# Kernel tuning notes

Hardware: AMD Instinct MI355X
Metric: run time of the kernel (lower is better)

Reference implementation:

```python
import jax, jax.numpy as jnp
import numpy as np

B, H, W, C = 64, 32, 32, 256
HZ, WZ = 16, 16
N = 64          # hidden_dim = n_proposals
K = 3           # dynamic depthwise kernel size
EPS = 1e-5


def _layernorm(x, g, b):
    mu = jnp.mean(x, axis=-1, keepdims=True)
    var = jnp.var(x, axis=-1, keepdims=True)
    return (x - mu) * jax.lax.rsqrt(var + EPS) * g + b


def setup_inputs() -> dict:
    key = jax.random.key(0)
    ks = jax.random.split(key, 8)
    s = 0.02  # weight init scale
    return {
        "x_feat": jax.random.normal(ks[0], (B, H, W, C), jnp.float32),
        "z_feat": jax.random.normal(ks[1], (B, HZ, WZ, C), jnp.float32),
        "Wz": jax.random.normal(ks[2], (C, N), jnp.float32) * s,
        "bz": jnp.zeros((N,), jnp.float32),
        "Wx": jax.random.normal(ks[3], (C, N), jnp.float32) * s,
        "bx": jnp.zeros((N,), jnp.float32),
        "Wdyn": jax.random.normal(ks[4], (C, N + K), jnp.float32) * s,
        "bdyn": jnp.zeros((N + K,), jnp.float32),
        "g_norm": jnp.ones((C,), jnp.float32),
        "b_norm": jnp.zeros((C,), jnp.float32),
        "Wp": jax.random.normal(ks[5], (C, 1), jnp.float32) * s,
        "bp": jnp.zeros((1,), jnp.float32),
        "g_ln": jnp.ones((C,), jnp.float32),
        "b_ln": jnp.zeros((C,), jnp.float32),
    }


def _dysep_conv_atten(query, value, Wdyn, bdyn, g_norm, b_norm):
    # query, value: [B, N, C]
    dy = query @ Wdyn + bdyn                      # [B, N, N+K]
    w_depth = dy[:, :, :K]                        # [B, N, K] per-channel depthwise kernels
    w_point = dy[:, :, K:]                        # [B, N, N] per-sample pointwise (1x1) weights
    # depthwise conv along C with 'same' padding (torch conv1d = cross-correlation)
    vpad = jnp.pad(value, ((0, 0), (0, 0), (1, 1)))
    depth = (w_depth[..., 0:1] * vpad[:, :, 0:C]
             + w_depth[..., 1:2] * vpad[:, :, 1:C + 1]
             + w_depth[..., 2:3] * vpad[:, :, 2:C + 2])
    depth = jax.nn.relu(depth)                    # [B, N, C]
    point = jnp.einsum('bnm,bmc->bnc', w_point, depth)
    return _layernorm(point, g_norm, b_norm)


def reference(x_feat, z_feat, Wz, bz, Wx, bx, Wdyn, bdyn,
              g_norm, b_norm, Wp, bp, g_ln, b_ln):
    # kernels from template features (detached in the original: kernels.detach())
    z_core = z_feat @ Wz + bz                                   # [B,HZ,WZ,N]
    kernels = jnp.einsum('bhwn,bhwc->bnc', z_core, z_feat)      # [B,N,C]
    kernels = jax.lax.stop_gradient(kernels)

    x_n = x_feat @ Wx + bx                                      # [B,H,W,N]
    kernels_x = jnp.einsum('bhwn,bhwc->bnc', x_n, x_feat)       # [B,N,C]
    kernels_x = _dysep_conv_atten(kernels, kernels_x, Wdyn, bdyn, g_norm, b_norm)

    x_corr = jnp.einsum('bnc,bhwn->bhwc', kernels_x, x_n)       # [B,H,W,C]
    proto = kernels_x @ Wp + bp                                 # [B,N,1]
    tem = jax.nn.sigmoid(jnp.einsum('bnd,bnc->bdc', proto, kernels_x))  # [B,1,C]
    tem = tem[:, :, None, :]                                    # [B,1,1,C]
    x_corr = x_corr * tem

    return x_feat + jax.nn.relu(_layernorm(x_corr, g_ln, b_ln))
```

## Files before the change

kernel.cpp:

```cpp
#include <hip/hip_runtime.h>
#include <math.h>

#define EPSV 1e-5f

__global__ __launch_bounds__(256) void gemm_all(
    const float* __restrict__ Xx, const float* __restrict__ Wxp,
    const float* __restrict__ bxp, float* __restrict__ Yx,
    const float* __restrict__ Xz, const float* __restrict__ Wzp,
    const float* __restrict__ bzp, float* __restrict__ Yz)
{
    __shared__ float Xc[16 * 132];
    __shared__ float Wc[16 * 64];
    const int t = threadIdx.x;
    const float *X, *W, *bias; float* Y; long r0;
    if (blockIdx.x < 512) { X = Xx; W = Wxp; bias = bxp; Y = Yx; r0 = (long)blockIdx.x * 128; }
    else                  { X = Xz; W = Wzp; bias = bzp; Y = Yz; r0 = (long)(blockIdx.x - 512) * 128; }

    const int tr = t >> 4, tc = t & 15;
    float4 bv = *(const float4*)(bias + tc * 4);
    float acc[8][4];
#pragma unroll
    for (int i = 0; i < 8; ++i) { acc[i][0]=bv.x; acc[i][1]=bv.y; acc[i][2]=bv.z; acc[i][3]=bv.w; }

    const int lr = t >> 2;
    const int lc = (t & 3) * 4;
    const int wl = t >> 4, wj = (t & 15) * 4;
    float4 xv0 = *(const float4*)(X + (r0 + lr) * 256 + lc);
    float4 xv1 = *(const float4*)(X + (r0 + lr + 64) * 256 + lc);
    float4 wv  = *(const float4*)(W + (long)wl * 64 + wj);

    for (int c0 = 0; c0 < 256; c0 += 16) {
        Xc[(lc+0)*132 + lr] = xv0.x; Xc[(lc+1)*132 + lr] = xv0.y;
        Xc[(lc+2)*132 + lr] = xv0.z; Xc[(lc+3)*132 + lr] = xv0.w;
        Xc[(lc+0)*132 + lr+64] = xv1.x; Xc[(lc+1)*132 + lr+64] = xv1.y;
        Xc[(lc+2)*132 + lr+64] = xv1.z; Xc[(lc+3)*132 + lr+64] = xv1.w;
        *(float4*)&Wc[wl * 64 + wj] = wv;
        __syncthreads();
        if (c0 + 16 < 256) {
            xv0 = *(const float4*)(X + (r0 + lr) * 256 + c0 + 16 + lc);
            xv1 = *(const float4*)(X + (r0 + lr + 64) * 256 + c0 + 16 + lc);
            wv  = *(const float4*)(W + (long)(c0 + 16 + wl) * 64 + wj);
        }
#pragma unroll
        for (int cl = 0; cl < 16; ++cl) {
            float4 a0 = *(float4*)&Xc[cl * 132 + tr * 8];
            float4 a1 = *(float4*)&Xc[cl * 132 + tr * 8 + 4];
            float4 b4 = *(float4*)&Wc[cl * 64 + tc * 4];
            acc[0][0]+=a0.x*b4.x; acc[0][1]+=a0.x*b4.y; acc[0][2]+=a0.x*b4.z; acc[0][3]+=a0.x*b4.w;
            acc[1][0]+=a0.y*b4.x; acc[1][1]+=a0.y*b4.y; acc[1][2]+=a0.y*b4.z; acc[1][3]+=a0.y*b4.w;
            acc[2][0]+=a0.z*b4.x; acc[2][1]+=a0.z*b4.y; acc[2][2]+=a0.z*b4.z; acc[2][3]+=a0.z*b4.w;
            acc[3][0]+=a0.w*b4.x; acc[3][1]+=a0.w*b4.y; acc[3][2]+=a0.w*b4.z; acc[3][3]+=a0.w*b4.w;
            acc[4][0]+=a1.x*b4.x; acc[4][1]+=a1.x*b4.y; acc[4][2]+=a1.x*b4.z; acc[4][3]+=a1.x*b4.w;
            acc[5][0]+=a1.y*b4.x; acc[5][1]+=a1.y*b4.y; acc[5][2]+=a1.y*b4.z; acc[5][3]+=a1.y*b4.w;
            acc[6][0]+=a1.z*b4.x; acc[6][1]+=a1.z*b4.y; acc[6][2]+=a1.z*b4.z; acc[6][3]+=a1.z*b4.w;
            acc[7][0]+=a1.w*b4.x; acc[7][1]+=a1.w*b4.y; acc[7][2]+=a1.w*b4.z; acc[7][3]+=a1.w*b4.w;
        }
        __syncthreads();
    }
#pragma unroll
    for (int i = 0; i < 8; ++i) {
        float4 o = make_float4(acc[i][0], acc[i][1], acc[i][2], acc[i][3]);
        *(float4*)(Y + (r0 + tr * 8 + i) * 64 + tc * 4) = o;
    }
}

__global__ __launch_bounds__(256) void corr_all(
    const float* __restrict__ xn, const float* __restrict__ xf,
    float* __restrict__ kxr, const float* __restrict__ zc,
    const float* __restrict__ zf, float* __restrict__ kern)
{
    __shared__ float A[64 * 64];
    __shared__ float Bt[64 * 64];
    const int t = threadIdx.x;
    const float *Yn, *X; float* S; int b, P;
    if (blockIdx.y < 64) { b = blockIdx.y;      Yn = xn; X = xf; S = kxr;  P = 1024; }
    else                 { b = blockIdx.y - 64; Yn = zc; X = zf; S = kern; P = 256;  }
    const int c0 = blockIdx.x * 64;
    const int tn = t >> 4, tc = t & 15;

    float acc[4][4] = {};
    float4 av[4], bv4[4];
#pragma unroll
    for (int i = 0; i < 4; ++i) {
        int idx = t + i * 256; int p = idx >> 4, f4 = (idx & 15) * 4;
        long rb = (long)b * P + p;
        av[i]  = *(const float4*)(Yn + rb * 64 + f4);
        bv4[i] = *(const float4*)(X + rb * 256 + c0 + f4);
    }
    for (int p0 = 0; p0 < P; p0 += 64) {
#pragma unroll
        for (int i = 0; i < 4; ++i) {
            int idx = t + i * 256; int p = idx >> 4, f4 = (idx & 15) * 4;
            *(float4*)&A[p * 64 + f4] = av[i];
            *(float4*)&Bt[p * 64 + f4] = bv4[i];
        }
        __syncthreads();
        if (p0 + 64 < P) {
#pragma unroll
            for (int i = 0; i < 4; ++i) {
                int idx = t + i * 256; int p = idx >> 4, f4 = (idx & 15) * 4;
                long rb = (long)b * P + p0 + 64 + p;
                av[i]  = *(const float4*)(Yn + rb * 64 + f4);
                bv4[i] = *(const float4*)(X + rb * 256 + c0 + f4);
            }
        }
#pragma unroll 16
        for (int p = 0; p < 64; ++p) {
            float4 a  = *(float4*)&A[p * 64 + tn * 4];
            float4 b4 = *(float4*)&Bt[p * 64 + tc * 4];
            acc[0][0]+=a.x*b4.x; acc[0][1]+=a.x*b4.y; acc[0][2]+=a.x*b4.z; acc[0][3]+=a.x*b4.w;
            acc[1][0]+=a.y*b4.x; acc[1][1]+=a.y*b4.y; acc[1][2]+=a.y*b4.z; acc[1][3]+=a.y*b4.w;
            acc[2][0]+=a.z*b4.x; acc[2][1]+=a.z*b4.y; acc[2][2]+=a.z*b4.z; acc[2][3]+=a.z*b4.w;
            acc[3][0]+=a.w*b4.x; acc[3][1]+=a.w*b4.y; acc[3][2]+=a.w*b4.z; acc[3][3]+=a.w*b4.w;
        }
        __syncthreads();
    }
#pragma unroll
    for (int i = 0; i < 4; ++i) {
        float4 o = make_float4(acc[i][0], acc[i][1], acc[i][2], acc[i][3]);
        *(float4*)(S + ((long)(b * 64 + tn * 4 + i)) * 256 + c0 + tc * 4) = o;
    }
}

__global__ __launch_bounds__(256) void dy_all(
    const float* __restrict__ kern, const float* __restrict__ Wdyn,
    const float* __restrict__ bdyn, float* __restrict__ dyb)
{
    __shared__ float Ac[16 * 64];
    __shared__ float Wc[16 * 64];
    __shared__ float Wd3[48];
    const int b = blockIdx.x, t = threadIdx.x;
    const int tr = t >> 4, tc = t & 15;
    float acc[4][4];
#pragma unroll
    for (int j = 0; j < 4; ++j) {
        float bj = bdyn[3 + tc * 4 + j];
        acc[0][j] = bj; acc[1][j] = bj; acc[2][j] = bj; acc[3][j] = bj;
    }
    const int lr = t >> 2, lc = (t & 3) * 4;
    const int wl = t >> 4, wj = (t & 15) * 4;
    const int nwd = t / 3, jwd = t - nwd * 3;
    float wdacc = 0.f;
    float4 av = *(const float4*)(kern + ((long)(b * 64 + lr)) * 256 + lc);
    float w0 = Wdyn[wl * 67 + 3 + wj + 0];
    float w1 = Wdyn[wl * 67 + 3 + wj + 1];
    float w2 = Wdyn[wl * 67 + 3 + wj + 2];
    float w3 = Wdyn[wl * 67 + 3 + wj + 3];
    float wdr = (t < 48) ? Wdyn[(t / 3) * 67 + (t % 3)] : 0.f;

    for (int c0 = 0; c0 < 256; c0 += 16) {
        Ac[(lc+0)*64 + lr] = av.x; Ac[(lc+1)*64 + lr] = av.y;
        Ac[(lc+2)*64 + lr] = av.z; Ac[(lc+3)*64 + lr] = av.w;
        Wc[wl*64 + wj+0] = w0; Wc[wl*64 + wj+1] = w1;
        Wc[wl*64 + wj+2] = w2; Wc[wl*64 + wj+3] = w3;
        if (t < 48) Wd3[t] = wdr;
        __syncthreads();
        if (c0 + 16 < 256) {
            av = *(const float4*)(kern + ((long)(b * 64 + lr)) * 256 + c0 + 16 + lc);
            w0 = Wdyn[(c0 + 16 + wl) * 67 + 3 + wj + 0];
            w1 = Wdyn[(c0 + 16 + wl) * 67 + 3 + wj + 1];
            w2 = Wdyn[(c0 + 16 + wl) * 67 + 3 + wj + 2];
            w3 = Wdyn[(c0 + 16 + wl) * 67 + 3 + wj + 3];
            if (t < 48) wdr = Wdyn[(c0 + 16 + t / 3) * 67 + (t % 3)];
        }
#pragma unroll
        for (int cl = 0; cl < 16; ++cl) {
            float4 a = *(float4*)&Ac[cl * 64 + tr * 4];
            float4 w = *(float4*)&Wc[cl * 64 + tc * 4];
            acc[0][0]+=a.x*w.x; acc[0][1]+=a.x*w.y; acc[0][2]+=a.x*w.z; acc[0][3]+=a.x*w.w;
            acc[1][0]+=a.y*w.x; acc[1][1]+=a.y*w.y; acc[1][2]+=a.y*w.z; acc[1][3]+=a.y*w.w;
            acc[2][0]+=a.z*w.x; acc[2][1]+=a.z*w.y; acc[2][2]+=a.z*w.z; acc[2][3]+=a.z*w.w;
            acc[3][0]+=a.w*w.x; acc[3][1]+=a.w*w.y; acc[3][2]+=a.w*w.z; acc[3][3]+=a.w*w.w;
        }
        if (t < 192) {
#pragma unroll
            for (int cl = 0; cl < 16; ++cl)
                wdacc += Ac[cl * 64 + nwd] * Wd3[cl * 3 + jwd];
        }
        __syncthreads();
    }
#pragma unroll
    for (int i = 0; i < 4; ++i) {
        float4 o = make_float4(acc[i][0], acc[i][1], acc[i][2], acc[i][3]);
        *(float4*)(dyb + ((long)(b * 64 + tr * 4 + i)) * 68 + tc * 4) = o;
    }
    if (t < 192) dyb[((long)(b * 64 + nwd)) * 68 + 64 + jwd] = wdacc + bdyn[jwd];
}

__global__ __launch_bounds__(256) void depthpoint(
    const float* __restrict__ dyb, const float* __restrict__ v,
    const float* __restrict__ g, const float* __restrict__ Wp,
    float* __restrict__ point, float* __restrict__ partials)
{
    __shared__ float smem[13312];
    float* wpT = smem;
    float* wd3 = smem + 4352;
    float* vt  = smem + 4608;
    float* dep = smem + 8960;
    float* rs  = vt;

    const int t = threadIdx.x;
    const int b = blockIdx.y, ct = blockIdx.x, c0 = ct * 64;
    const int tr = t >> 4, tc = t & 15;

#pragma unroll
    for (int i = 0; i < 4; ++i) {
        int idx = t + i * 256; int n = idx >> 4, m0 = (idx & 15) * 4;
        float4 w4 = *(const float4*)(dyb + ((long)(b * 64 + n)) * 68 + m0);
        wpT[(m0+0)*68 + n] = w4.x; wpT[(m0+1)*68 + n] = w4.y;
        wpT[(m0+2)*68 + n] = w4.z; wpT[(m0+3)*68 + n] = w4.w;
    }
    if (t < 64) {
        long o = ((long)(b * 64 + t)) * 68 + 64;
        wd3[t*4+0] = dyb[o+0]; wd3[t*4+1] = dyb[o+1]; wd3[t*4+2] = dyb[o+2];
    }
    {
        int m = t >> 2, lc0 = (t & 3) * 17;
#pragma unroll
        for (int k = 0; k < 17; ++k) {
            int lc = lc0 + k;
            if (lc < 66) {
                int c = c0 - 1 + lc;
                vt[m * 68 + lc] = (c >= 0 && c < 256) ? v[((long)(b * 64 + m)) * 256 + c] : 0.f;
            }
        }
    }
    __syncthreads();
#pragma unroll
    for (int im = 0; im < 4; ++im) {
        int m = tr * 4 + im;
        float w0 = wd3[m*4+0], w1 = wd3[m*4+1], w2 = wd3[m*4+2];
#pragma unroll
        for (int jc = 0; jc < 4; ++jc) {
            int cl = tc * 4 + jc;
            float d = w0 * vt[m*68 + cl] + w1 * vt[m*68 + cl + 1] + w2 * vt[m*68 + cl + 2];
            dep[m*68 + cl] = fmaxf(d, 0.f);
        }
    }
    __syncthreads();
    float acc[4][4] = {};
#pragma unroll 16
    for (int m = 0; m < 64; ++m) {
        float4 a4 = *(float4*)&wpT[m * 68 + tr * 4];
        float4 d4 = *(float4*)&dep[m * 68 + tc * 4];
        acc[0][0]+=a4.x*d4.x; acc[0][1]+=a4.x*d4.y; acc[0][2]+=a4.x*d4.z; acc[0][3]+=a4.x*d4.w;
        acc[1][0]+=a4.y*d4.x; acc[1][1]+=a4.y*d4.y; acc[1][2]+=a4.y*d4.z; acc[1][3]+=a4.y*d4.w;
        acc[2][0]+=a4.z*d4.x; acc[2][1]+=a4.z*d4.y; acc[2][2]+=a4.z*d4.z; acc[2][3]+=a4.z*d4.w;
        acc[3][0]+=a4.w*d4.x; acc[3][1]+=a4.w*d4.y; acc[3][2]+=a4.w*d4.z; acc[3][3]+=a4.w*d4.w;
    }
    int cg = c0 + tc * 4;
    float4 g4  = *(const float4*)(g + cg);
    float4 wp4 = *(const float4*)(Wp + cg);
    float gw0 = g4.x*wp4.x, gw1 = g4.y*wp4.y, gw2 = g4.z*wp4.z, gw3 = g4.w*wp4.w;
#pragma unroll
    for (int i = 0; i < 4; ++i) {
        float4 o = make_float4(acc[i][0], acc[i][1], acc[i][2], acc[i][3]);
        *(float4*)(point + ((long)(b * 64 + tr * 4 + i)) * 256 + cg) = o;
        float s  = o.x + o.y + o.z + o.w;
        float s2 = o.x*o.x + o.y*o.y + o.z*o.z + o.w*o.w;
        float dg = o.x*gw0 + o.y*gw1 + o.z*gw2 + o.w*gw3;
        rs[0*1088 + (tr*4+i)*17 + tc] = s;
        rs[1*1088 + (tr*4+i)*17 + tc] = s2;
        rs[2*1088 + (tr*4+i)*17 + tc] = dg;
    }
    __syncthreads();
    if (t < 64) {
        float s = 0.f, s2 = 0.f, dg = 0.f;
#pragma unroll
        for (int j = 0; j < 16; ++j) {
            s  += rs[t*17 + j];
            s2 += rs[1088 + t*17 + j];
            dg += rs[2176 + t*17 + j];
        }
        long base = ((long)(b * 4 + ct)) * 192;
        partials[base + t]        = s;
        partials[base + 64 + t]   = s2;
        partials[base + 128 + t]  = dg;
    }
}

__global__ __launch_bounds__(256) void lntem(
    const float* __restrict__ partials, const float* __restrict__ point,
    const float* __restrict__ g, const float* __restrict__ bta,
    const float* __restrict__ Wp, const float* __restrict__ bp,
    float* __restrict__ murr, float* __restrict__ AB)
{
    __shared__ float sA[256], sB[256];
    __shared__ float wnv[64];
    __shared__ float tot[4];
    const int b = blockIdx.x, t = threadIdx.x;
    const int c = t;
    float gc = g[c], bc = bta[c], wpc = Wp[c];
    sA[t] = gc * wpc; sB[t] = bc * wpc;
    __syncthreads();
    for (int off = 128; off >= 1; off >>= 1) {
        if (t < off) { sA[t] += sA[t+off]; sB[t] += sB[t+off]; }
        __syncthreads();
    }
    if (t == 0) { tot[0] = sA[0]; tot[1] = sB[0] + bp[0]; }
    __syncthreads();
    float Sgw = tot[0], Sbw = tot[1];

    float protoe = 0.f, mu = 0.f, rr = 0.f;
    if (t < 64) {
        float S1 = 0.f, S2 = 0.f, Sdg = 0.f;
#pragma unroll
        for (int ct = 0; ct < 4; ++ct) {
            long o = ((long)(b * 4 + ct)) * 192;
            S1 += partials[o + t]; S2 += partials[o + 64 + t]; Sdg += partials[o + 128 + t];
        }
        mu = S1 * (1.f / 256.f);
        float var = S2 * (1.f / 256.f) - mu * mu;
        rr = rsqrtf(var + EPSV);
        protoe = rr * (Sdg - mu * Sgw) + Sbw;
        wnv[t] = protoe * rr;
        murr[b * 128 + 2*t]     = rr;
        murr[b * 128 + 2*t + 1] = -mu * rr;
    }
    __syncthreads();
    sA[t] = (t < 64) ? protoe * rr * mu : 0.f;
    sB[t] = (t < 64) ? protoe : 0.f;
    __syncthreads();
    for (int off = 128; off >= 1; off >>= 1) {
        if (t < off) { sA[t] += sA[t+off]; sB[t] += sB[t+off]; }
        __syncthreads();
    }
    if (t == 0) { tot[2] = sA[0]; tot[3] = sB[0]; }
    __syncthreads();
    float Bv = tot[2], Sv = tot[3];

    const float* pcol = point + (long)b * 64 * 256 + c;
    float a0 = 0.f, a1 = 0.f, a2 = 0.f, a3 = 0.f;
#pragma unroll
    for (int n = 0; n < 64; n += 4) {
        a0 += wnv[n+0] * pcol[(n+0) * 256];
        a1 += wnv[n+1] * pcol[(n+1) * 256];
        a2 += wnv[n+2] * pcol[(n+2) * 256];
        a3 += wnv[n+3] * pcol[(n+3) * 256];
    }
    float accA = a0 + a1 + a2 + a3;
    float x = gc * (accA - Bv) + bc * Sv;
    float temv = 1.f / (1.f + expf(-x));
    AB[b * 512 + c]       = gc * temv;
    AB[b * 512 + 256 + c] = bc * temv;
}

__global__ __launch_bounds__(256) void final_kernel(
    const float* __restrict__ xn, const float* __restrict__ point,
    const float* __restrict__ murr, const float* __restrict__ AB,
    const float* __restrict__ xf, const float* __restrict__ g,
    const float* __restrict__ bt, float* __restrict__ out)
{
    __shared__ float xtT[64 * 68];
    __shared__ float kc[64 * 68];
    __shared__ float rs1[64 * 17], rs2[64 * 17];
    __shared__ float mu[64], rr[64];
    __shared__ float rq[128];
    const int t = threadIdx.x;
    const int b = blockIdx.y;
    const int pg = blockIdx.x;
    const int tr = t >> 4;
    const int tc = t & 15;

    if (t < 128) rq[t] = murr[b * 128 + t];
    {
        int row = t >> 2, q = t & 3;
        const float* src = xn + ((long)(b * 1024 + pg * 64 + row)) * 64 + q * 16;
        float4 f0 = *(const float4*)(src + 0);
        float4 f1 = *(const float4*)(src + 4);
        float4 f2 = *(const float4*)(src + 8);
        float4 f3 = *(const float4*)(src + 12);
        int n0 = q * 16;
        xtT[(n0+ 0)*68+row]=f0.x; xtT[(n0+ 1)*68+row]=f0.y; xtT[(n0+ 2)*68+row]=f0.z; xtT[(n0+ 3)*68+row]=f0.w;
        xtT[(n0+ 4)*68+row]=f1.x; xtT[(n0+ 5)*68+row]=f1.y; xtT[(n0+ 6)*68+row]=f1.z; xtT[(n0+ 7)*68+row]=f1.w;
        xtT[(n0+ 8)*68+row]=f2.x; xtT[(n0+ 9)*68+row]=f2.y; xtT[(n0+10)*68+row]=f2.z; xtT[(n0+11)*68+row]=f2.w;
        xtT[(n0+12)*68+row]=f3.x; xtT[(n0+13)*68+row]=f3.y; xtT[(n0+14)*68+row]=f3.z; xtT[(n0+15)*68+row]=f3.w;
    }

    float4 xcv[4][4];
    float si[4] = {0.f,0.f,0.f,0.f}, s2i[4] = {0.f,0.f,0.f,0.f};
#pragma unroll
    for (int cc = 0; cc < 4; ++cc) {
        __syncthreads();
#pragma unroll
        for (int i = 0; i < 4; ++i) {
            int idx = t + i * 256;
            int n = idx >> 4, jq = idx & 15;
            int cb = cc * 64 + jq * 4;
            float4 p4 = *(const float4*)(point + ((long)(b * 64 + n)) * 256 + cb);
            float rn = rq[2*n], qn = rq[2*n + 1];
            float4 A4 = *(const float4*)(AB + b * 512 + cb);
            float4 B4 = *(const float4*)(AB + b * 512 + 256 + cb);
            float4 kv;
            kv.x = (p4.x * rn + qn) * A4.x + B4.x;
            kv.y = (p4.y * rn + qn) * A4.y + B4.y;
            kv.z = (p4.z * rn + qn) * A4.z + B4.z;
            kv.w = (p4.w * rn + qn) * A4.w + B4.w;
            *(float4*)&kc[n * 68 + jq * 4] = kv;
        }
        __syncthreads();
        float4 a0 = {0,0,0,0}, a1 = {0,0,0,0}, a2 = {0,0,0,0}, a3 = {0,0,0,0};
#pragma unroll 8
        for (int n = 0; n < 64; ++n) {
            float4 xv = *(float4*)&xtT[n * 68 + tr * 4];
            float4 kv = *(float4*)&kc[n * 68 + tc * 4];
            a0.x += xv.x*kv.x; a0.y += xv.x*kv.y; a0.z += xv.x*kv.z; a0.w += xv.x*kv.w;
            a1.x += xv.y*kv.x; a1.y += xv.y*kv.y; a1.z += xv.y*kv.z; a1.w += xv.y*kv.w;
            a2.x += xv.z*kv.x; a2.y += xv.z*kv.y; a2.z += xv.z*kv.z; a2.w += xv.z*kv.w;
            a3.x += xv.w*kv.x; a3.y += xv.w*kv.y; a3.z += xv.w*kv.z; a3.w += xv.w*kv.w;
        }
        xcv[cc][0] = a0; xcv[cc][1] = a1; xcv[cc][2] = a2; xcv[cc][3] = a3;
        si[0] += a0.x+a0.y+a0.z+a0.w;  s2i[0] += a0.x*a0.x+a0.y*a0.y+a0.z*a0.z+a0.w*a0.w;
        si[1] += a1.x+a1.y+a1.z+a1.w;  s2i[1] += a1.x*a1.x+a1.y*a1.y+a1.z*a1.z+a1.w*a1.w;
        si[2] += a2.x+a2.y+a2.z+a2.w;  s2i[2] += a2.x*a2.x+a2.y*a2.y+a2.z*a2.z+a2.w*a2.w;
        si[3] += a3.x+a3.y+a3.z+a3.w;  s2i[3] += a3.x*a3.x+a3.y*a3.y+a3.z*a3.z+a3.w*a3.w;
    }
#pragma unroll
    for (int i = 0; i < 4; ++i) { rs1[(tr*4+i)*17 + tc] = si[i]; rs2[(tr*4+i)*17 + tc] = s2i[i]; }
    __syncthreads();
    if (t < 64) {
        float s = 0.f, s2 = 0.f;
#pragma unroll
        for (int k = 0; k < 16; ++k) { s += rs1[t*17 + k]; s2 += rs2[t*17 + k]; }
        float m = s * (1.f / 256.f);
        mu[t] = m; rr[t] = rsqrtf(s2 * (1.f / 256.f) - m * m + EPSV);
    }
    __syncthreads();
#pragma unroll
    for (int cc = 0; cc < 4; ++cc) {
        int cb = cc * 64 + tc * 4;
        float4 g4 = *(const float4*)(g + cb);
        float4 b4 = *(const float4*)(bt + cb);
#pragma unroll
        for (int i = 0; i < 4; ++i) {
            int row = tr * 4 + i;
            float m = mu[row], r = rr[row];
            long grow = ((long)(b * 1024 + pg * 64 + row)) * 256;
            float4 xfv = *(const float4*)(xf + grow + cb);
            float4 a = xcv[cc][i];
            float4 o;
            o.x = xfv.x + fmaxf((a.x - m) * r * g4.x + b4.x, 0.f);
            o.y = xfv.y + fmaxf((a.y - m) * r * g4.y + b4.y, 0.f);
            o.z = xfv.z + fmaxf((a.z - m) * r * g4.z + b4.z, 0.f);
            o.w = xfv.w + fmaxf((a.w - m) * r * g4.w + b4.w, 0.f);
            *(float4*)(out + grow + cb) = o;
        }
    }
}

extern "C" void kernel_launch(void* const* d_in, const int* in_sizes, int n_in,
                              void* d_out, int out_size, void* d_ws, size_t ws_size,
                              hipStream_t stream)
{
    (void)in_sizes; (void)n_in; (void)out_size; (void)ws_size;
    const float* x_feat = (const float*)d_in[0];
    const float* z_feat = (const float*)d_in[1];
    const float* Wz     = (const float*)d_in[2];
    const float* bz     = (const float*)d_in[3];
    const float* Wx     = (const float*)d_in[4];
    const float* bx     = (const float*)d_in[5];
    const float* Wdyn   = (const float*)d_in[6];
    const float* bdyn   = (const float*)d_in[7];
    const float* g_norm = (const float*)d_in[8];
    const float* b_norm = (const float*)d_in[9];
    const float* Wp     = (const float*)d_in[10];
    const float* bp     = (const float*)d_in[11];
    const float* g_ln   = (const float*)d_in[12];
    const float* b_ln   = (const float*)d_in[13];
    float* out = (float*)d_out;

    float* ws       = (float*)d_ws;
    float* xn       = ws;
    float* zc       = xn + 4194304;
    float* kern     = zc + 1048576;
    float* kxr      = kern + 1048576;
    float* point    = kxr + 1048576;
    float* dyb      = point + 1048576;
    float* partials = dyb + 278528;
    float* murr     = partials + 49152;
    float* AB       = murr + 8192;

    gemm_all<<<640, 256, 0, stream>>>(x_feat, Wx, bx, xn, z_feat, Wz, bz, zc);
    corr_all<<<dim3(4, 128), 256, 0, stream>>>(xn, x_feat, kxr, zc, z_feat, kern);
    dy_all<<<64, 256, 0, stream>>>(kern, Wdyn, bdyn, dyb);
    depthpoint<<<dim3(4, 64), 256, 0, stream>>>(dyb, kxr, g_norm, Wp, point, partials);
    lntem<<<64, 256, 0, stream>>>(partials, point, g_norm, b_norm, Wp, bp, murr, AB);
    final_kernel<<<dim3(16, 64), 256, 0, stream>>>(xn, point, murr, AB, x_feat, g_ln, b_ln, out);
}
```

Measured before the change: 324.6 us.

## Run correlation GEMMs on bf16 MFMA with transposed operands emitted by projection GEMM

The projection GEMM now also writes bf16, K-major (transposed) copies of the projected features and the raw input features. A new correlation kernel consumes these copies through 16x16x32 bf16 MFMA instructions instead of the fp32 FMA loop. This targets the compute cost of the correlation GEMM over the spatial dimension and halves its operand bytes, at the price of extra bf16 writes from the first kernel and reduced precision in the kernel/correlation results.

```diff
diff --git a/kernel.cpp b/kernel.cpp
--- a/kernel.cpp
+++ b/kernel.cpp
@@ -2,19 +2,44 @@
 #include <math.h>
 
 #define EPSV 1e-5f
+
+typedef __attribute__((ext_vector_type(8))) short short8;
+typedef __attribute__((ext_vector_type(4))) float f32x4;
+
+static __device__ __forceinline__ unsigned bfpack2(float lo, float hi) {
+    union { float f; unsigned u; } a, b;
+    a.f = lo; b.f = hi;
+    unsigned ua = a.u + 0x7fffu + ((a.u >> 16) & 1u);
+    unsigned ub = b.u + 0x7fffu + ((b.u >> 16) & 1u);
+    return (ua >> 16) | (ub & 0xffff0000u);
+}
 
 __global__ __launch_bounds__(256) void gemm_all(
     const float* __restrict__ Xx, const float* __restrict__ Wxp,
     const float* __restrict__ bxp, float* __restrict__ Yx,
     const float* __restrict__ Xz, const float* __restrict__ Wzp,
-    const float* __restrict__ bzp, float* __restrict__ Yz)
+    const float* __restrict__ bzp,
+    unsigned short* __restrict__ xnbT, unsigned short* __restrict__ xfbT,
+    unsigned short* __restrict__ zcbT, unsigned short* __restrict__ zfbT)
 {
     __shared__ float Xc[16 * 132];
     __shared__ float Wc[16 * 64];
     const int t = threadIdx.x;
-    const float *X, *W, *bias; float* Y; long r0;
-    if (blockIdx.x < 512) { X = Xx; W = Wxp; bias = bxp; Y = Yx; r0 = (long)blockIdx.x * 128; }
-    else                  { X = Xz; W = Wzp; bias = bzp; Y = Yz; r0 = (long)(blockIdx.x - 512) * 128; }
+    const float *X, *W, *bias; float* Y;
+    unsigned short *Tn, *Tf;
+    long r0; int P, bb, p0;
+    if (blockIdx.x < 512) {
+        X = Xx; W = Wxp; bias = bxp; Y = Yx;
+        r0 = (long)blockIdx.x * 128;
+        P = 1024; bb = blockIdx.x >> 3; p0 = (blockIdx.x & 7) * 128;
+        Tn = xnbT; Tf = xfbT;
+    } else {
+        int zb = blockIdx.x - 512;
+        X = Xz; W = Wzp; bias = bzp; Y = nullptr;
+        r0 = (long)zb * 128;
+        P = 256; bb = zb >> 1; p0 = (zb & 1) * 128;
+        Tn = zcbT; Tf = zfbT;
+    }
 
     const int tr = t >> 4, tc = t & 15;
     float4 bv = *(const float4*)(bias + tc * 4);
@@ -55,70 +80,101 @@
             acc[6][0]+=a1.z*b4.x; acc[6][1]+=a1.z*b4.y; acc[6][2]+=a1.z*b4.z; acc[6][3]+=a1.z*b4.w;
             acc[7][0]+=a1.w*b4.x; acc[7][1]+=a1.w*b4.y; acc[7][2]+=a1.w*b4.z; acc[7][3]+=a1.w*b4.w;
         }
-        __syncthreads();
-    }
-#pragma unroll
-    for (int i = 0; i < 8; ++i) {
-        float4 o = make_float4(acc[i][0], acc[i][1], acc[i][2], acc[i][3]);
-        *(float4*)(Y + (r0 + tr * 8 + i) * 64 + tc * 4) = o;
-    }
-}
-
-__global__ __launch_bounds__(256) void corr_all(
-    const float* __restrict__ xn, const float* __restrict__ xf,
-    float* __restrict__ kxr, const float* __restrict__ zc,
-    const float* __restrict__ zf, float* __restrict__ kern)
-{
-    __shared__ float A[64 * 64];
-    __shared__ float Bt[64 * 64];
+        {
+            int cl2 = t >> 4, p8 = (t & 15) * 8;
+            const float* xr = &Xc[cl2 * 132 + p8];
+            uint4 pk;
+            pk.x = bfpack2(xr[0], xr[1]); pk.y = bfpack2(xr[2], xr[3]);
+            pk.z = bfpack2(xr[4], xr[5]); pk.w = bfpack2(xr[6], xr[7]);
+            *(uint4*)(Tf + ((long)(bb * 256 + c0 + cl2)) * P + p0 + p8) = pk;
+        }
+        __syncthreads();
+    }
+    if (Y) {
+#pragma unroll
+        for (int i = 0; i < 8; ++i) {
+            float4 o = make_float4(acc[i][0], acc[i][1], acc[i][2], acc[i][3]);
+            *(float4*)(Y + (r0 + tr * 8 + i) * 64 + tc * 4) = o;
+        }
+    }
+#pragma unroll
+    for (int j = 0; j < 4; ++j) {
+        int n = tc * 4 + j;
+        uint4 pk;
+        pk.x = bfpack2(acc[0][j], acc[1][j]);
+        pk.y = bfpack2(acc[2][j], acc[3][j]);
+        pk.z = bfpack2(acc[4][j], acc[5][j]);
+        pk.w = bfpack2(acc[6][j], acc[7][j]);
+        *(uint4*)(Tn + ((long)(bb * 64 + n)) * P + p0 + tr * 8) = pk;
+    }
+}
+
+__global__ __launch_bounds__(256) void corr_mfma(
+    const unsigned short* __restrict__ xnbT, const unsigned short* __restrict__ xfbT,
+    float* __restrict__ kxr,
+    const unsigned short* __restrict__ zcbT, const unsigned short* __restrict__ zfbT,
+    float* __restrict__ kern)
+{
+    __shared__ __align__(16) unsigned short AT[64 * 136];
+    __shared__ __align__(16) unsigned short BT[64 * 136];
     const int t = threadIdx.x;
-    const float *Yn, *X; float* S; int b, P;
-    if (blockIdx.y < 64) { b = blockIdx.y;      Yn = xn; X = xf; S = kxr;  P = 1024; }
-    else                 { b = blockIdx.y - 64; Yn = zc; X = zf; S = kern; P = 256;  }
-    const int c0 = blockIdx.x * 64;
-    const int tn = t >> 4, tc = t & 15;
-
-    float acc[4][4] = {};
-    float4 av[4], bv4[4];
+    const unsigned short *Ab, *Bb; float* S; int b, P;
+    if (blockIdx.y < 64) { b = blockIdx.y;      Ab = xnbT; Bb = xfbT; S = kxr;  P = 1024; }
+    else                 { b = blockIdx.y - 64; Ab = zcbT; Bb = zfbT; S = kern; P = 256;  }
+    const int ct = blockIdx.x;
+    const int w = t >> 6, l = t & 63;
+    const int quad = l >> 4, lane16 = l & 15;
+
+    const unsigned short* Abase = Ab + (long)b * 64 * P;
+    const unsigned short* Bbase = Bb + ((long)(b * 256 + ct * 64)) * P;
+    const int srow = t >> 4, sk = (t & 15) * 8;
+
+    f32x4 acc[4] = {{0.f,0.f,0.f,0.f},{0.f,0.f,0.f,0.f},{0.f,0.f,0.f,0.f},{0.f,0.f,0.f,0.f}};
+
+    uint4 pa[4], pb[4];
 #pragma unroll
     for (int i = 0; i < 4; ++i) {
-        int idx = t + i * 256; int p = idx >> 4, f4 = (idx & 15) * 4;
-        long rb = (long)b * P + p;
-        av[i]  = *(const float4*)(Yn + rb * 64 + f4);
-        bv4[i] = *(const float4*)(X + rb * 256 + c0 + f4);
-    }
-    for (int p0 = 0; p0 < P; p0 += 64) {
+        int row = srow + i * 16;
+        pa[i] = *(const uint4*)(Abase + (long)row * P + sk);
+        pb[i] = *(const uint4*)(Bbase + (long)row * P + sk);
+    }
+    const int nk = P >> 7;
+    for (int kc = 0; kc < nk; ++kc) {
 #pragma unroll
         for (int i = 0; i < 4; ++i) {
-            int idx = t + i * 256; int p = idx >> 4, f4 = (idx & 15) * 4;
-            *(float4*)&A[p * 64 + f4] = av[i];
-            *(float4*)&Bt[p * 64 + f4] = bv4[i];
-        }
-        __syncthreads();
-        if (p0 + 64 < P) {
+            int row = srow + i * 16;
+            *(uint4*)&AT[row * 136 + sk] = pa[i];
+            *(uint4*)&BT[row * 136 + sk] = pb[i];
+        }
+        __syncthreads();
+        if (kc + 1 < nk) {
+            int ko = (kc + 1) * 128 + sk;
 #pragma unroll
             for (int i = 0; i < 4; ++i) {
-                int idx = t + i * 256; int p = idx >> 4, f4 = (idx & 15) * 4;
-                long rb = (long)b * P + p0 + 64 + p;
-                av[i]  = *(const float4*)(Yn + rb * 64 + f4);
-                bv4[i] = *(const float4*)(X + rb * 256 + c0 + f4);
+                int row = srow + i * 16;
+                pa[i] = *(const uint4*)(Abase + (long)row * P + ko);
+                pb[i] = *(const uint4*)(Bbase + (long)row * P + ko);
             }
         }
-#pragma unroll 16
-        for (int p = 0; p < 64; ++p) {
-            float4 a  = *(float4*)&A[p * 64 + tn * 4];
-            float4 b4 = *(float4*)&Bt[p * 64 + tc * 4];
-            acc[0][0]+=a.x*b4.x; acc[0][1]+=a.x*b4.y; acc[0][2]+=a.x*b4.z; acc[0][3]+=a.x*b4.w;
-            acc[1][0]+=a.y*b4.x; acc[1][1]+=a.y*b4.y; acc[1][2]+=a.y*b4.z; acc[1][3]+=a.y*b4.w;
-            acc[2][0]+=a.z*b4.x; acc[2][1]+=a.z*b4.y; acc[2][2]+=a.z*b4.z; acc[2][3]+=a.z*b4.w;
-            acc[3][0]+=a.w*b4.x; acc[3][1]+=a.w*b4.y; acc[3][2]+=a.w*b4.z; acc[3][3]+=a.w*b4.w;
-        }
-        __syncthreads();
-    }
-#pragma unroll
-    for (int i = 0; i < 4; ++i) {
-        float4 o = make_float4(acc[i][0], acc[i][1], acc[i][2], acc[i][3]);
-        *(float4*)(S + ((long)(b * 64 + tn * 4 + i)) * 256 + c0 + tc * 4) = o;
+#pragma unroll
+        for (int ks = 0; ks < 4; ++ks) {
+            const int ko2 = ks * 32 + quad * 8;
+            short8 bfrag = *(const short8*)&BT[(w * 16 + lane16) * 136 + ko2];
+#pragma unroll
+            for (int mi = 0; mi < 4; ++mi) {
+                short8 afrag = *(const short8*)&AT[(mi * 16 + lane16) * 136 + ko2];
+                acc[mi] = __builtin_amdgcn_mfma_f32_16x16x32_bf16(afrag, bfrag, acc[mi], 0, 0, 0);
+            }
+        }
+        __syncthreads();
+    }
+#pragma unroll
+    for (int mi = 0; mi < 4; ++mi) {
+        long row = (long)(b * 64 + mi * 16 + quad * 4);
+        int col = ct * 64 + w * 16 + lane16;
+#pragma unroll
+        for (int r = 0; r < 4; ++r)
+            S[(row + r) * 256 + col] = acc[mi][r];
     }
 }
 
@@ -471,17 +527,21 @@
 
     float* ws       = (float*)d_ws;
     float* xn       = ws;
-    float* zc       = xn + 4194304;
-    float* kern     = zc + 1048576;
+    float* kern     = xn + 4194304;
     float* kxr      = kern + 1048576;
     float* point    = kxr + 1048576;
     float* dyb      = point + 1048576;
     float* partials = dyb + 278528;
     float* murr     = partials + 49152;
     float* AB       = murr + 8192;
-
-    gemm_all<<<640, 256, 0, stream>>>(x_feat, Wx, bx, xn, z_feat, Wz, bz, zc);
-    corr_all<<<dim3(4, 128), 256, 0, stream>>>(xn, x_feat, kxr, zc, z_feat, kern);
+    unsigned short* xnbT = (unsigned short*)(AB + 32768);
+    unsigned short* xfbT = xnbT + 4194304;
+    unsigned short* zcbT = xfbT + 16777216;
+    unsigned short* zfbT = zcbT + 1048576;
+
+    gemm_all<<<640, 256, 0, stream>>>(x_feat, Wx, bx, xn, z_feat, Wz, bz,
+                                      xnbT, xfbT, zcbT, zfbT);
+    corr_mfma<<<dim3(4, 128), 256, 0, stream>>>(xnbT, xfbT, kxr, zcbT, zfbT, kern);
     dy_all<<<64, 256, 0, stream>>>(kern, Wdyn, bdyn, dyb);
     depthpoint<<<dim3(4, 64), 256, 0, stream>>>(dyb, kxr, g_norm, Wp, point, partials);
     lntem<<<64, 256, 0, stream>>>(partials, point, g_norm, b_norm, Wp, bp, murr, AB);
```

Measured after the change: 287.9 us. -11.3%, faster.
